# Kernel optimization log

Measured on AMD Instinct MI355X. Metric: run time of the kernel, lower is better.

The kernel has to match this reference:

```python
import jax, jax.numpy as jnp
import numpy as np

HEAD = 16  # from init_kwargs
NEG_FILL = -1e20


def setup_inputs() -> dict:
    key = jax.random.key(0)
    ks = jax.random.split(key, 6)
    N, S, E = 4, 2048, 1024
    D = E // HEAD  # 64
    value = jax.random.normal(ks[0], (N, S, E), dtype=jnp.float32)
    key_t = jax.random.normal(ks[1], (N, S, E), dtype=jnp.float32)
    query = jax.random.normal(ks[2], (N, S, E), dtype=jnp.float32)
    # multiplicative causal mask broadcastable to (N, H, S, S)
    mask = jnp.tril(jnp.ones((S, S), dtype=jnp.float32))[None, None, :, :]
    # per-head-dim projection weights (Dense(head_dim) applied after reshape,
    # so weights are (D, D), shared across heads) -- faithful to source
    sc = 1.0 / np.sqrt(D)
    Wq = jax.random.normal(ks[3], (D, D), dtype=jnp.float32) * sc
    Wk = jax.random.normal(ks[4], (D, D), dtype=jnp.float32) * sc
    Wv = jax.random.normal(ks[5], (D, D), dtype=jnp.float32) * sc
    return {"value": value, "key": key_t, "query": query, "mask": mask,
            "Wq": Wq, "Wk": Wk, "Wv": Wv}


def reference(value, key, query, mask, Wq, Wk, Wv):
    N, Lq, E = query.shape
    H = HEAD
    D = E // H
    # reshape to heads, then project last dim (D -> D)
    q = jnp.einsum('nqhd,de->nqhe', query.reshape(N, Lq, H, D), Wq)
    k = jnp.einsum('nkhd,de->nkhe', key.reshape(N, key.shape[1], H, D), Wk)
    v = jnp.einsum('nvhd,de->nvhe', value.reshape(N, value.shape[1], H, D), Wv)
    # unscaled QK^T (source has no 1/sqrt(d))
    energy = jnp.einsum('nqhd,nkhd->nhqk', q, k)  # (N,H,Lq,Lk)
    energy = energy * mask
    energy = jnp.where(energy == 0, NEG_FILL, energy)
    attention = jax.nn.softmax(energy, axis=-1)
    out = jnp.einsum('nhql,nlhd->nqhd', attention, v).reshape(N, Lq, H * D)
    return out  # fc_layer defined in __init__ but never used in call()
```

## Files before the change

### kernel.cpp

```cpp
#include <hip/hip_runtime.h>
#include <hip/hip_bf16.h>
#include <math.h>


#define NB  4
#define SEQ 2048
#define HD  16
#define DH  64
#define NH  (NB*HD)

typedef _Float16 half8  __attribute__((ext_vector_type(8)));
typedef _Float16 half2  __attribute__((ext_vector_type(2)));
typedef __fp16   fp16x2 __attribute__((ext_vector_type(2)));
typedef float    f32x4  __attribute__((ext_vector_type(4)));
typedef float    f32x16 __attribute__((ext_vector_type(16)));

__device__ inline half2 pkrtz(float a, float b) {
  union { fp16x2 f; half2 h; } u;
  u.f = __builtin_amdgcn_cvt_pkrtz(a, b);
  return u.h;
}

__device__ inline void gload16(const void* g, void* l) {
  __builtin_amdgcn_global_load_lds(
      (const __attribute__((address_space(1))) void*)g,
      (__attribute__((address_space(3))) void*)l, 16, 0, 0);
}

__global__ __launch_bounds__(256) void proj_kernel(
    const float* __restrict__ q_in, const float* __restrict__ k_in,
    const float* __restrict__ v_in,
    const float* __restrict__ Wq, const float* __restrict__ Wk,
    const float* __restrict__ Wv,
    _Float16* __restrict__ Qp, _Float16* __restrict__ Kp,
    _Float16* __restrict__ Vt)
{
  __shared__ float Wl[64*64];
  const int t = threadIdx.x;
  const int which = blockIdx.z;
  const float* in = which == 0 ? q_in : (which == 1 ? k_in : v_in);
  const float* W  = which == 0 ? Wq   : (which == 1 ? Wk   : Wv);

  const int nh = blockIdx.y;
  const int n = nh >> 4, h = nh & 15;
  const int s0 = blockIdx.x * 256;

  #pragma unroll
  for (int i = 0; i < 16; ++i) Wl[i*256 + t] = W[i*256 + t];
  __syncthreads();

  const int w = t >> 6, lane = t & 63, lr = lane & 15, lg = lane >> 4;

  if (which < 2) {
    half8 bfr[4][2];
    #pragma unroll
    for (int g = 0; g < 4; ++g)
      #pragma unroll
      for (int kc = 0; kc < 2; ++kc)
        #pragma unroll
        for (int i = 0; i < 8; ++i)
          bfr[g][kc][i] = (_Float16)Wl[(kc*32 + lg*8 + i)*64 + 16*g + lr];

    _Float16* outp = (which == 0 ? Qp : Kp) + (size_t)nh*SEQ*DH;
    #pragma unroll
    for (int pass = 0; pass < 4; ++pass) {
      int row0 = s0 + (pass*4 + w)*16;
      const float* ip = in + ((size_t)(n*SEQ + row0 + lr))*(HD*DH) + h*DH;
      float4 a0 = *(const float4*)(ip + lg*8);
      float4 a1 = *(const float4*)(ip + lg*8 + 4);
      float4 a2 = *(const float4*)(ip + 32 + lg*8);
      float4 a3 = *(const float4*)(ip + 32 + lg*8 + 4);
      half8 af0, af1;
      af0[0]=(_Float16)a0.x; af0[1]=(_Float16)a0.y; af0[2]=(_Float16)a0.z; af0[3]=(_Float16)a0.w;
      af0[4]=(_Float16)a1.x; af0[5]=(_Float16)a1.y; af0[6]=(_Float16)a1.z; af0[7]=(_Float16)a1.w;
      af1[0]=(_Float16)a2.x; af1[1]=(_Float16)a2.y; af1[2]=(_Float16)a2.z; af1[3]=(_Float16)a2.w;
      af1[4]=(_Float16)a3.x; af1[5]=(_Float16)a3.y; af1[6]=(_Float16)a3.z; af1[7]=(_Float16)a3.w;
      f32x4 c[4] = {{0,0,0,0},{0,0,0,0},{0,0,0,0},{0,0,0,0}};
      #pragma unroll
      for (int g = 0; g < 4; ++g) {
        c[g] = __builtin_amdgcn_mfma_f32_16x16x32_f16(af0, bfr[g][0], c[g], 0, 0, 0);
        c[g] = __builtin_amdgcn_mfma_f32_16x16x32_f16(af1, bfr[g][1], c[g], 0, 0, 0);
      }
      #pragma unroll
      for (int g = 0; g < 4; ++g)
        #pragma unroll
        for (int j = 0; j < 4; ++j)
          outp[(size_t)(row0 + 4*lg + j)*DH + 16*g + lr] = (_Float16)c[g][j];
    }
  } else {
    half8 afr[2];
    #pragma unroll
    for (int kc = 0; kc < 2; ++kc)
      #pragma unroll
      for (int i = 0; i < 8; ++i)
        afr[kc][i] = (_Float16)Wl[(kc*32 + lg*8 + i)*64 + w*16 + lr];

    _Float16* outp = Vt + (size_t)nh*DH*SEQ;
    #pragma unroll
    for (int pass = 0; pass < 4; ++pass) {
      int sc0 = s0 + pass*64;
      f32x4 c[4] = {{0,0,0,0},{0,0,0,0},{0,0,0,0},{0,0,0,0}};
      #pragma unroll
      for (int g = 0; g < 4; ++g) {
        const float* ip = in + ((size_t)(n*SEQ + sc0 + 16*g + lr))*(HD*DH) + h*DH;
        float4 b0 = *(const float4*)(ip + lg*8);
        float4 b1 = *(const float4*)(ip + lg*8 + 4);
        float4 b2 = *(const float4*)(ip + 32 + lg*8);
        float4 b3 = *(const float4*)(ip + 32 + lg*8 + 4);
        half8 bf0, bf1;
        bf0[0]=(_Float16)b0.x; bf0[1]=(_Float16)b0.y; bf0[2]=(_Float16)b0.z; bf0[3]=(_Float16)b0.w;
        bf0[4]=(_Float16)b1.x; bf0[5]=(_Float16)b1.y; bf0[6]=(_Float16)b1.z; bf0[7]=(_Float16)b1.w;
        bf1[0]=(_Float16)b2.x; bf1[1]=(_Float16)b2.y; bf1[2]=(_Float16)b2.z; bf1[3]=(_Float16)b2.w;
        bf1[4]=(_Float16)b3.x; bf1[5]=(_Float16)b3.y; bf1[6]=(_Float16)b3.z; bf1[7]=(_Float16)b3.w;
        c[g] = __builtin_amdgcn_mfma_f32_16x16x32_f16(afr[0], bf0, c[g], 0, 0, 0);
        c[g] = __builtin_amdgcn_mfma_f32_16x16x32_f16(afr[1], bf1, c[g], 0, 0, 0);
      }
      #pragma unroll
      for (int g = 0; g < 4; ++g)
        #pragma unroll
        for (int j = 0; j < 4; ++j) {
          int kcol = 16*g + lr;
          int pcol = (kcol & ~12) | ((kcol & 8) >> 1) | ((kcol & 4) << 1);
          outp[(size_t)(w*16 + 4*lg + j)*SEQ + sc0 + pcol] = (_Float16)c[g][j];
        }
    }
  }
}

__global__ __launch_bounds__(256) void attn_kernel(
    const _Float16* __restrict__ Qp,
    const _Float16* __restrict__ Kp,
    const _Float16* __restrict__ Vt,
    float* __restrict__ out)
{
  __shared__ __attribute__((aligned(16))) _Float16 Kl[2][64*64];
  __shared__ __attribute__((aligned(16))) _Float16 Vl[2][64*64];

  const int nh = blockIdx.y;
  const int n = nh >> 4, h = nh & 15;
  const int sb = ((blockIdx.y >> 4) & 1) ? (int)blockIdx.x : (15 - (int)blockIdx.x);
  const int qs = sb * 128;
  const int tid = threadIdx.x;
  const int w = tid >> 6, lane = tid & 63;
  const int lq = lane & 31, lg1 = lane >> 5;
  const int q0 = qs + w*32;
  const int q  = q0 + lq;

  const _Float16* Kbase = Kp + (size_t)nh*SEQ*DH;
  const _Float16* Vbase = Vt + (size_t)nh*DH*SEQ;

  const _Float16* Qrow = Qp + ((size_t)nh*SEQ + q)*DH + 8*lg1;
  half8 qf[4];
  #pragma unroll
  for (int c = 0; c < 4; ++c) qf[c] = *(const half8*)(Qrow + 16*c);

  int roff[2][4];
  #pragma unroll
  for (int rt = 0; rt < 2; ++rt)
    #pragma unroll
    for (int c = 0; c < 4; ++c)
      roff[rt][c] = (32*rt + lq)*128 + (((2*c + lg1) ^ (lq & 7)) << 4);

  const int srow = tid >> 3;
  const int scs  = (tid & 7) ^ (srow & 7);
  const _Float16* kg = Kbase + (size_t)srow*DH + scs*8;
  const _Float16* vg = Vbase + (size_t)srow*SEQ + scs*8;

  float m = -INFINITY, lsum = 0.f;
  f32x16 o0 = {0,0,0,0,0,0,0,0,0,0,0,0,0,0,0,0};
  f32x16 o1 = {0,0,0,0,0,0,0,0,0,0,0,0,0,0,0,0};

  const int Tw   = q0 >> 6;
  const int Tmax = 2*sb + 1;

  gload16(kg,            &Kl[0][tid*8]);
  gload16(kg + 32*DH,    &Kl[0][(256+tid)*8]);
  gload16(vg,            &Vl[0][tid*8]);
  gload16(vg + 32*SEQ,   &Vl[0][(256+tid)*8]);

  int cur = 0;
  for (int t = 0; t <= Tmax; ++t) {
    if (t < Tmax) {
      const _Float16* kgt = kg + (size_t)(t+1)*64*DH;
      const _Float16* vgt = vg + (t+1)*64;
      _Float16* kd = &Kl[cur^1][0];
      _Float16* vd = &Vl[cur^1][0];
      gload16(kgt,          kd + tid*8);
      gload16(kgt + 32*DH,  kd + (256+tid)*8);
      gload16(vgt,          vd + tid*8);
      gload16(vgt + 32*SEQ, vd + (256+tid)*8);
      asm volatile("s_waitcnt vmcnt(4)" ::: "memory");
    } else {
      asm volatile("s_waitcnt vmcnt(0)" ::: "memory");
    }
    __builtin_amdgcn_sched_barrier(0);
    __builtin_amdgcn_s_barrier();
    __builtin_amdgcn_sched_barrier(0);

    if (t <= Tw) {
      const char* Kb = (const char*)&Kl[cur][0];
      const char* Vb = (const char*)&Vl[cur][0];
      const int kt = t*64;

      f32x16 s0 = {0,0,0,0,0,0,0,0,0,0,0,0,0,0,0,0};
      f32x16 s1 = {0,0,0,0,0,0,0,0,0,0,0,0,0,0,0,0};
      #pragma unroll
      for (int c = 0; c < 4; ++c) {
        half8 ka = *(const half8*)(Kb + roff[0][c]);
        half8 kb = *(const half8*)(Kb + roff[1][c]);
        s0 = __builtin_amdgcn_mfma_f32_32x32x16_f16(ka, qf[c], s0, 0, 0, 0);
        s1 = __builtin_amdgcn_mfma_f32_32x32x16_f16(kb, qf[c], s1, 0, 0, 0);
      }
      if (t == Tw) {
        #pragma unroll
        for (int j = 0; j < 16; ++j) {
          int kl = 4*lg1 + 8*(j>>2) + (j&3);
          if (kt + kl      > q) s0[j] = -1e30f;
          if (kt + 32 + kl > q) s1[j] = -1e30f;
        }
      }
      float t0[8];
      #pragma unroll
      for (int j = 0; j < 8; ++j)
        t0[j] = fmaxf(fmaxf(s0[j], s0[j+8]), fmaxf(s1[j], s1[j+8]));
      float pm = fmaxf(fmaxf(fmaxf(t0[0],t0[1]), fmaxf(t0[2],t0[3])),
                       fmaxf(fmaxf(t0[4],t0[5]), fmaxf(t0[6],t0[7])));
      pm = fmaxf(pm, __shfl_xor(pm, 32));
      float mn = fmaxf(m, pm);
      float sc = __expf(m - mn);
      m = mn;
      #pragma unroll
      for (int j = 0; j < 16; ++j) {
        s0[j] = __expf(s0[j] - m);
        s1[j] = __expf(s1[j] - m);
      }
      float u0[8];
      #pragma unroll
      for (int j = 0; j < 8; ++j)
        u0[j] = (s0[j] + s0[j+8]) + (s1[j] + s1[j+8]);
      float ps = ((u0[0]+u0[1]) + (u0[2]+u0[3])) + ((u0[4]+u0[5]) + (u0[6]+u0[7]));
      ps += __shfl_xor(ps, 32);
      lsum = lsum*sc + ps;
      #pragma unroll
      for (int j = 0; j < 16; ++j) { o0[j] *= sc; o1[j] *= sc; }

      half2 pkA[8], pkB[8];
      #pragma unroll
      for (int jj = 0; jj < 8; ++jj) {
        pkA[jj] = pkrtz(s0[2*jj], s0[2*jj+1]);
        pkB[jj] = pkrtz(s1[2*jj], s1[2*jj+1]);
      }
      #pragma unroll
      for (int c = 0; c < 4; ++c) {
        union { half8 h; half2 p[4]; } pb;
        pb.p[0] = (c < 2) ? pkA[(c&1)*4 + 0] : pkB[(c&1)*4 + 0];
        pb.p[1] = (c < 2) ? pkA[(c&1)*4 + 1] : pkB[(c&1)*4 + 1];
        pb.p[2] = (c < 2) ? pkA[(c&1)*4 + 2] : pkB[(c&1)*4 + 2];
        pb.p[3] = (c < 2) ? pkA[(c&1)*4 + 3] : pkB[(c&1)*4 + 3];
        half8 va = *(const half8*)(Vb + roff[0][c]);
        half8 vb = *(const half8*)(Vb + roff[1][c]);
        o0 = __builtin_amdgcn_mfma_f32_32x32x16_f16(va, pb.h, o0, 0, 0, 0);
        o1 = __builtin_amdgcn_mfma_f32_32x32x16_f16(vb, pb.h, o1, 0, 0, 0);
      }
    }

    __builtin_amdgcn_sched_barrier(0);
    __builtin_amdgcn_s_barrier();
    cur ^= 1;
  }

  float inv = 1.0f / lsum;
  float* orow = out + ((size_t)n*SEQ + q)*(HD*DH) + h*DH;
  #pragma unroll
  for (int j = 0; j < 16; ++j) {
    int dl = 4*lg1 + 8*(j>>2) + (j&3);
    orow[dl]      = o0[j] * inv;
    orow[32 + dl] = o1[j] * inv;
  }
}

extern "C" void kernel_launch(void* const* d_in, const int* in_sizes, int n_in,
                              void* d_out, int out_size, void* d_ws, size_t ws_size,
                              hipStream_t stream) {
  (void)in_sizes; (void)n_in; (void)out_size; (void)ws_size;
  const float* value = (const float*)d_in[0];
  const float* key   = (const float*)d_in[1];
  const float* query = (const float*)d_in[2];
  const float* Wq = (const float*)d_in[4];
  const float* Wk = (const float*)d_in[5];
  const float* Wv = (const float*)d_in[6];

  _Float16* Qp = (_Float16*)d_ws;
  _Float16* Kp = Qp + (size_t)NH*SEQ*DH;
  _Float16* Vt = Kp + (size_t)NH*SEQ*DH;
  float* out = (float*)d_out;

  proj_kernel<<<dim3(8, 64, 3), 256, 0, stream>>>(query, key, value,
                                                  Wq, Wk, Wv, Qp, Kp, Vt);
  attn_kernel<<<dim3(16, 64), 256, 0, stream>>>(Qp, Kp, Vt, out);
}
```

Baseline: 127.5 us.

## Pair causal query blocks per workgroup, fold log2e into Q, add lazy rescale

Each attention workgroup now handles two query blocks, p and 15-p, one after the other, so every block does the same amount of causal work; the grid shrinks to 8x64. Q is pre-scaled by log2(e) in the projection so the kernel can use exp2f. The online-softmax rescale is skipped while the new max stays within 8 of the running max. s_setprio is raised around the MFMA sections. The changes trade fewer, longer workgroups (512 blocks total) for less tail imbalance, and the lazy rescale allows unnormalised exponents up to about 2^8 in fp16.

```diff
diff --git a/kernel.cpp b/kernel.cpp
--- a/kernel.cpp
+++ b/kernel.cpp
@@ -52,6 +52,7 @@
   const int w = t >> 6, lane = t & 63, lr = lane & 15, lg = lane >> 4;
 
   if (which < 2) {
+    const float oscale = (which == 0) ? 1.44269504088896f : 1.0f;
     half8 bfr[4][2];
     #pragma unroll
     for (int g = 0; g < 4; ++g)
@@ -85,7 +86,8 @@
       for (int g = 0; g < 4; ++g)
         #pragma unroll
         for (int j = 0; j < 4; ++j)
-          outp[(size_t)(row0 + 4*lg + j)*DH + 16*g + lr] = (_Float16)c[g][j];
+          outp[(size_t)(row0 + 4*lg + j)*DH + 16*g + lr] =
+              (_Float16)(c[g][j] * oscale);
     }
   } else {
     half8 afr[2];
@@ -127,6 +129,14 @@
   }
 }
 
+#define STAGE(kd, vd, ktn)                                        \
+  do {                                                            \
+    gload16(kg + (size_t)(ktn)*DH, (kd) + tid*8);                 \
+    gload16(kg + (size_t)(ktn)*DH + 32*DH, (kd) + (256+tid)*8);   \
+    gload16(vg + (ktn), (vd) + tid*8);                            \
+    gload16(vg + (ktn) + 32*SEQ, (vd) + (256+tid)*8);             \
+  } while (0)
+
 __global__ __launch_bounds__(256) void attn_kernel(
     const _Float16* __restrict__ Qp,
     const _Float16* __restrict__ Kp,
@@ -136,23 +146,29 @@
   __shared__ __attribute__((aligned(16))) _Float16 Kl[2][64*64];
   __shared__ __attribute__((aligned(16))) _Float16 Vl[2][64*64];
 
-  const int nh = blockIdx.y;
-  const int n = nh >> 4, h = nh & 15;
-  const int sb = ((blockIdx.y >> 4) & 1) ? (int)blockIdx.x : (15 - (int)blockIdx.x);
-  const int qs = sb * 128;
+  const int head = blockIdx.y;
+  const int n = head >> 4, h = head & 15;
+  const int p  = blockIdx.x;
   const int tid = threadIdx.x;
   const int w = tid >> 6, lane = tid & 63;
   const int lq = lane & 31, lg1 = lane >> 5;
-  const int q0 = qs + w*32;
-  const int q  = q0 + lq;
-
-  const _Float16* Kbase = Kp + (size_t)nh*SEQ*DH;
-  const _Float16* Vbase = Vt + (size_t)nh*DH*SEQ;
-
-  const _Float16* Qrow = Qp + ((size_t)nh*SEQ + q)*DH + 8*lg1;
+
+  const int TmaxA = 2*p + 1;
+  const int TmaxB = 31 - 2*p;
+  const int q0A = p*128 + w*32;
+  const int q0B = (15 - p)*128 + w*32;
+  const int TwA = q0A >> 6;
+  const int TwB = q0B >> 6;
+  const int G   = TmaxA + TmaxB + 2;
+
+  const _Float16* Kbase = Kp + (size_t)head*SEQ*DH;
+  const _Float16* Vbase = Vt + (size_t)head*DH*SEQ;
+
+  const _Float16* QrowA = Qp + ((size_t)head*SEQ + q0A + lq)*DH + 8*lg1;
+  const _Float16* QrowB = Qp + ((size_t)head*SEQ + q0B + lq)*DH + 8*lg1;
   half8 qf[4];
   #pragma unroll
-  for (int c = 0; c < 4; ++c) qf[c] = *(const half8*)(Qrow + 16*c);
+  for (int c = 0; c < 4; ++c) qf[c] = *(const half8*)(QrowA + 16*c);
 
   int roff[2][4];
   #pragma unroll
@@ -170,25 +186,18 @@
   f32x16 o0 = {0,0,0,0,0,0,0,0,0,0,0,0,0,0,0,0};
   f32x16 o1 = {0,0,0,0,0,0,0,0,0,0,0,0,0,0,0,0};
 
-  const int Tw   = q0 >> 6;
-  const int Tmax = 2*sb + 1;
-
-  gload16(kg,            &Kl[0][tid*8]);
-  gload16(kg + 32*DH,    &Kl[0][(256+tid)*8]);
-  gload16(vg,            &Vl[0][tid*8]);
-  gload16(vg + 32*SEQ,   &Vl[0][(256+tid)*8]);
+  STAGE(&Kl[0][0], &Vl[0][0], 0);
 
   int cur = 0;
-  for (int t = 0; t <= Tmax; ++t) {
-    if (t < Tmax) {
-      const _Float16* kgt = kg + (size_t)(t+1)*64*DH;
-      const _Float16* vgt = vg + (t+1)*64;
-      _Float16* kd = &Kl[cur^1][0];
-      _Float16* vd = &Vl[cur^1][0];
-      gload16(kgt,          kd + tid*8);
-      gload16(kgt + 32*DH,  kd + (256+tid)*8);
-      gload16(vgt,          vd + tid*8);
-      gload16(vgt + 32*SEQ, vd + (256+tid)*8);
+  for (int g = 0; g < G; ++g) {
+    const bool phA = (g <= TmaxA);
+    const int  tt  = phA ? g : (g - TmaxA - 1);
+    const int  Tw  = phA ? TwA : TwB;
+
+    if (g + 1 < G) {
+      const int gn  = g + 1;
+      const int ktn = (gn <= TmaxA ? gn : (gn - TmaxA - 1)) * 64;
+      STAGE(&Kl[cur^1][0], &Vl[cur^1][0], ktn);
       asm volatile("s_waitcnt vmcnt(4)" ::: "memory");
     } else {
       asm volatile("s_waitcnt vmcnt(0)" ::: "memory");
@@ -197,13 +206,15 @@
     __builtin_amdgcn_s_barrier();
     __builtin_amdgcn_sched_barrier(0);
 
-    if (t <= Tw) {
+    if (tt <= Tw) {
       const char* Kb = (const char*)&Kl[cur][0];
       const char* Vb = (const char*)&Vl[cur][0];
-      const int kt = t*64;
+      const int kt = tt*64;
+      const int q  = (phA ? q0A : q0B) + lq;
 
       f32x16 s0 = {0,0,0,0,0,0,0,0,0,0,0,0,0,0,0,0};
       f32x16 s1 = {0,0,0,0,0,0,0,0,0,0,0,0,0,0,0,0};
+      __builtin_amdgcn_s_setprio(1);
       #pragma unroll
       for (int c = 0; c < 4; ++c) {
         half8 ka = *(const half8*)(Kb + roff[0][c]);
@@ -211,7 +222,8 @@
         s0 = __builtin_amdgcn_mfma_f32_32x32x16_f16(ka, qf[c], s0, 0, 0, 0);
         s1 = __builtin_amdgcn_mfma_f32_32x32x16_f16(kb, qf[c], s1, 0, 0, 0);
       }
-      if (t == Tw) {
+      __builtin_amdgcn_s_setprio(0);
+      if (tt == Tw) {
         #pragma unroll
         for (int j = 0; j < 16; ++j) {
           int kl = 4*lg1 + 8*(j>>2) + (j&3);
@@ -226,13 +238,18 @@
       float pm = fmaxf(fmaxf(fmaxf(t0[0],t0[1]), fmaxf(t0[2],t0[3])),
                        fmaxf(fmaxf(t0[4],t0[5]), fmaxf(t0[6],t0[7])));
       pm = fmaxf(pm, __shfl_xor(pm, 32));
-      float mn = fmaxf(m, pm);
-      float sc = __expf(m - mn);
-      m = mn;
+      if (!__all(pm <= m + 8.f)) {
+        float mn = fmaxf(m, pm);
+        float sc = exp2f(m - mn);
+        m = mn;
+        lsum *= sc;
+        #pragma unroll
+        for (int j = 0; j < 16; ++j) { o0[j] *= sc; o1[j] *= sc; }
+      }
       #pragma unroll
       for (int j = 0; j < 16; ++j) {
-        s0[j] = __expf(s0[j] - m);
-        s1[j] = __expf(s1[j] - m);
+        s0[j] = exp2f(s0[j] - m);
+        s1[j] = exp2f(s1[j] - m);
       }
       float u0[8];
       #pragma unroll
@@ -240,9 +257,7 @@
         u0[j] = (s0[j] + s0[j+8]) + (s1[j] + s1[j+8]);
       float ps = ((u0[0]+u0[1]) + (u0[2]+u0[3])) + ((u0[4]+u0[5]) + (u0[6]+u0[7]));
       ps += __shfl_xor(ps, 32);
-      lsum = lsum*sc + ps;
-      #pragma unroll
-      for (int j = 0; j < 16; ++j) { o0[j] *= sc; o1[j] *= sc; }
+      lsum += ps;
 
       half2 pkA[8], pkB[8];
       #pragma unroll
@@ -250,27 +265,45 @@
         pkA[jj] = pkrtz(s0[2*jj], s0[2*jj+1]);
         pkB[jj] = pkrtz(s1[2*jj], s1[2*jj+1]);
       }
+      __builtin_amdgcn_s_setprio(1);
       #pragma unroll
       for (int c = 0; c < 4; ++c) {
-        union { half8 h; half2 p[4]; } pb;
-        pb.p[0] = (c < 2) ? pkA[(c&1)*4 + 0] : pkB[(c&1)*4 + 0];
-        pb.p[1] = (c < 2) ? pkA[(c&1)*4 + 1] : pkB[(c&1)*4 + 1];
-        pb.p[2] = (c < 2) ? pkA[(c&1)*4 + 2] : pkB[(c&1)*4 + 2];
-        pb.p[3] = (c < 2) ? pkA[(c&1)*4 + 3] : pkB[(c&1)*4 + 3];
+        union { half8 hh; half2 pp[4]; } pb;
+        pb.pp[0] = (c < 2) ? pkA[(c&1)*4 + 0] : pkB[(c&1)*4 + 0];
+        pb.pp[1] = (c < 2) ? pkA[(c&1)*4 + 1] : pkB[(c&1)*4 + 1];
+        pb.pp[2] = (c < 2) ? pkA[(c&1)*4 + 2] : pkB[(c&1)*4 + 2];
+        pb.pp[3] = (c < 2) ? pkA[(c&1)*4 + 3] : pkB[(c&1)*4 + 3];
         half8 va = *(const half8*)(Vb + roff[0][c]);
         half8 vb = *(const half8*)(Vb + roff[1][c]);
-        o0 = __builtin_amdgcn_mfma_f32_32x32x16_f16(va, pb.h, o0, 0, 0, 0);
-        o1 = __builtin_amdgcn_mfma_f32_32x32x16_f16(vb, pb.h, o1, 0, 0, 0);
-      }
+        o0 = __builtin_amdgcn_mfma_f32_32x32x16_f16(va, pb.hh, o0, 0, 0, 0);
+        o1 = __builtin_amdgcn_mfma_f32_32x32x16_f16(vb, pb.hh, o1, 0, 0, 0);
+      }
+      __builtin_amdgcn_s_setprio(0);
     }
 
     __builtin_amdgcn_sched_barrier(0);
     __builtin_amdgcn_s_barrier();
+
+    if (g == TmaxA) {
+      float inv = 1.0f / lsum;
+      float* orow = out + ((size_t)n*SEQ + q0A + lq)*(HD*DH) + h*DH;
+      #pragma unroll
+      for (int j = 0; j < 16; ++j) {
+        int dl = 4*lg1 + 8*(j>>2) + (j&3);
+        orow[dl]      = o0[j] * inv;
+        orow[32 + dl] = o1[j] * inv;
+      }
+      m = -INFINITY; lsum = 0.f;
+      #pragma unroll
+      for (int j = 0; j < 16; ++j) { o0[j] = 0.f; o1[j] = 0.f; }
+      #pragma unroll
+      for (int c = 0; c < 4; ++c) qf[c] = *(const half8*)(QrowB + 16*c);
+    }
     cur ^= 1;
   }
 
   float inv = 1.0f / lsum;
-  float* orow = out + ((size_t)n*SEQ + q)*(HD*DH) + h*DH;
+  float* orow = out + ((size_t)n*SEQ + q0B + lq)*(HD*DH) + h*DH;
   #pragma unroll
   for (int j = 0; j < 16; ++j) {
     int dl = 4*lg1 + 8*(j>>2) + (j&3);
@@ -297,5 +330,5 @@
 
   proj_kernel<<<dim3(8, 64, 3), 256, 0, stream>>>(query, key, value,
                                                   Wq, Wk, Wv, Qp, Kp, Vt);
-  attn_kernel<<<dim3(16, 64), 256, 0, stream>>>(Qp, Kp, Vt, out);
-}
+  attn_kernel<<<dim3(8, 64), 256, 0, stream>>>(Qp, Kp, Vt, out);
+}
```

New measurement: 126.4 us. Within noise of the previous version (-0.9%).
